# Kernel optimization log

Hardware: AMD Instinct MI355X
Metric: run time of the kernel (lower is better)

## Reference

```python
import jax, jax.numpy as jnp
import numpy as np

B, S, D = 4, 2048, 1024
H, HD = 16, 64
DFF = 4096
EPS = 1e-6


def setup_inputs() -> dict:
    key = jax.random.key(0)
    ks = jax.random.split(key, 16)
    sc = 0.02
    def w(k, shape):
        return jax.random.normal(k, shape, dtype=jnp.float32) * sc
    return {
        'x': jax.random.normal(ks[0], (B, S, D), dtype=jnp.float32),
        'wq': w(ks[1], (D, D)), 'bq': jnp.zeros((D,), jnp.float32),
        'wk': w(ks[2], (D, D)), 'bk': jnp.zeros((D,), jnp.float32),
        'wv': w(ks[3], (D, D)), 'bv': jnp.zeros((D,), jnp.float32),
        'wo': w(ks[4], (D, D)), 'bo': jnp.zeros((D,), jnp.float32),
        'w1': w(ks[5], (D, DFF)), 'b1': jnp.zeros((DFF,), jnp.float32),
        'w2': w(ks[6], (DFF, D)), 'b2': jnp.zeros((D,), jnp.float32),
        'ln1_a': jnp.ones((D,), jnp.float32), 'ln1_b': jnp.zeros((D,), jnp.float32),
        'ln2_a': jnp.ones((D,), jnp.float32), 'ln2_b': jnp.zeros((D,), jnp.float32),
    }


def layernorm(x, alpha, bias):
    # Matches torch module: std is unbiased (ddof=1), divide by (std + eps)
    mean = jnp.mean(x, axis=-1, keepdims=True)
    var = jnp.sum((x - mean) ** 2, axis=-1, keepdims=True) / (x.shape[-1] - 1)
    std = jnp.sqrt(var)
    return alpha * ((x - mean) / (std + EPS)) + bias


def mha(x, wq, bq, wk, bk, wv, bv, wo, bo):
    q = (x @ wq + bq).reshape(B, S, H, HD)
    k = (x @ wk + bk).reshape(B, S, H, HD)
    v = (x @ wv + bv).reshape(B, S, H, HD)
    scores = jnp.einsum('bqhd,bkhd->bhqk', q, k) / jnp.sqrt(jnp.float32(HD))
    attn = jax.nn.softmax(scores, axis=-1)
    out = jnp.einsum('bhqk,bkhd->bqhd', attn, v).reshape(B, S, D)
    return out @ wo + bo


def reference(x, wq, bq, wk, bk, wv, bv, wo, bo, w1, b1, w2, b2,
              ln1_a, ln1_b, ln2_a, ln2_b):
    # Residual 1: x + MHA(LN(x))   (dropout = identity, eval mode)
    x = x + mha(layernorm(x, ln1_a, ln1_b), wq, bq, wk, bk, wv, bv, wo, bo)
    # Residual 2: x + FFN(LN(x))
    h = layernorm(x, ln2_a, ln2_b)
    ffn = jax.nn.relu(h @ w1 + b1) @ w2 + b2
    return x + ffn
```

## Files before the change

### kernel.cpp

```cpp
#include <hip/hip_runtime.h>

#define S_ 2048
#define D_ 1024

typedef unsigned short u16;
typedef unsigned int u32;
typedef __bf16 bf16x8 __attribute__((ext_vector_type(8)));
typedef unsigned short us8 __attribute__((ext_vector_type(8)));
typedef unsigned short us4 __attribute__((ext_vector_type(4)));
typedef unsigned int u32x4 __attribute__((ext_vector_type(4)));
typedef float f32x4 __attribute__((ext_vector_type(4)));

#if __has_builtin(__builtin_amdgcn_exp2f)
#define EXP2(x) __builtin_amdgcn_exp2f(x)
#else
#define EXP2(x) exp2f(x)
#endif

static __device__ __forceinline__ u16 f2bf(float f) {
  unsigned u = __builtin_bit_cast(unsigned, f);
  u += 0x7fffu + ((u >> 16) & 1u);
  return (u16)(u >> 16);
}

static __device__ __forceinline__ float bf2f(u16 h) {
  return __builtin_bit_cast(float, (u32)h << 16);
}

static __device__ __forceinline__ unsigned cvtpk_bf16(float lo, float hi) {
  unsigned r;
  asm("v_cvt_pk_bf16_f32 %0, %1, %2" : "=v"(r) : "v"(lo), "v"(hi));
  return r;
}

static __device__ __forceinline__ f32x4 mfma16(bf16x8 a, bf16x8 b, f32x4 c) {
  return __builtin_amdgcn_mfma_f32_16x16x32_bf16(a, b, c, 0, 0, 0);
}

static __device__ __forceinline__ void gload16(const void* g, void* lds) {
  __builtin_amdgcn_global_load_lds((const __attribute__((address_space(1))) void*)g,
                                   (__attribute__((address_space(3))) void*)lds, 16, 0, 0);
}

__global__ __launch_bounds__(256) void prep_kernel(
    const float* __restrict__ x, u16* __restrict__ xA, const float* __restrict__ ln1a,
    const float* __restrict__ ln1b, const float* __restrict__ wq, const float* __restrict__ wk,
    const float* __restrict__ wv, const float* __restrict__ wo, const float* __restrict__ w1,
    const float* __restrict__ w2, const float* __restrict__ bq, const float* __restrict__ bk,
    const float* __restrict__ bv, u16* __restrict__ wqkv, u16* __restrict__ wot,
    u16* __restrict__ w1t, u16* __restrict__ w2t, float* __restrict__ bcat, float qs) {
  const int bid = blockIdx.x;
  const int tx = threadIdx.x, ty = threadIdx.y;
  const int tid = ty * 32 + tx;
  if (bid < 8192) {
    const int row = bid;
    const float4 v = *(const float4*)(x + (size_t)row * D_ + tid * 4);
    float s = v.x + v.y + v.z + v.w;
    float ss = v.x * v.x + v.y * v.y + v.z * v.z + v.w * v.w;
#pragma unroll
    for (int off = 32; off >= 1; off >>= 1) {
      s += __shfl_xor(s, off);
      ss += __shfl_xor(ss, off);
    }
    __shared__ float red[8];
    const int w = tid >> 6, lane = tid & 63;
    if (lane == 0) { red[w] = s; red[4 + w] = ss; }
    __syncthreads();
    s = red[0] + red[1] + red[2] + red[3];
    ss = red[4] + red[5] + red[6] + red[7];
    const float mean = s * (1.0f / D_);
    const float var = (ss - s * mean) * (1.0f / (D_ - 1));
    const float inv = 1.0f / (sqrtf(var) + 1e-6f);
    const int j = tid * 4;
    const float4 av = *(const float4*)(ln1a + j);
    const float4 bv = *(const float4*)(ln1b + j);
    us4 o;
    o[0] = f2bf((v.x - mean) * inv * av.x + bv.x);
    o[1] = f2bf((v.y - mean) * inv * av.y + bv.y);
    o[2] = f2bf((v.z - mean) * inv * av.z + bv.z);
    o[3] = f2bf((v.w - mean) * inv * av.w + bv.w);
    *(us4*)(xA + (size_t)row * D_ + j) = o;
    return;
  }
  if (bid >= 20480) {
    const int i = (bid - 20480) * 256 + tid;
    bcat[i] = (i < 1024) ? bq[i] * qs : ((i < 2048) ? bk[i - 1024] : bv[i - 2048]);
    return;
  }
  const int tb = bid - 8192;
  const float* in;
  u16* out;
  int K, N, idx;
  float sc = 1.0f;
  if (tb < 4096) {
    K = 1024; N = 1024; idx = tb & 1023;
    if (tb < 1024)      { in = wq; out = wqkv;             sc = qs; }
    else if (tb < 2048) { in = wk; out = wqkv + (1 << 20); }
    else if (tb < 3072) { in = wv; out = wqkv + (2 << 20); }
    else                { in = wo; out = wot; }
  } else if (tb < 8192) {
    in = w1; out = w1t; K = 1024; N = 4096; idx = tb - 4096;
  } else {
    in = w2; out = w2t; K = 4096; N = 1024; idx = tb - 8192;
  }
  const int nb = N >> 5;
  const int n0 = (idx % nb) * 32, k0 = (idx / nb) * 32;
  __shared__ float t[32][33];
#pragma unroll
  for (int i = 0; i < 4; i++)
    t[ty + 8 * i][tx] = in[(size_t)(k0 + ty + 8 * i) * N + n0 + tx];
  __syncthreads();
#pragma unroll
  for (int i = 0; i < 4; i++)
    out[(size_t)(n0 + ty + 8 * i) * K + k0 + tx] = f2bf(t[tx][ty + 8 * i] * sc);
}

__global__ __launch_bounds__(256) void ln_bf16_kernel(const u16* __restrict__ in,
                                                      u16* __restrict__ out,
                                                      const float* __restrict__ alpha,
                                                      const float* __restrict__ beta) {
  const int row = blockIdx.x;
  const int tid = threadIdx.x;
  const us4 h = *(const us4*)(in + (size_t)row * D_ + tid * 4);
  float v0 = bf2f(h[0]), v1 = bf2f(h[1]), v2 = bf2f(h[2]), v3 = bf2f(h[3]);
  float s = v0 + v1 + v2 + v3;
  float ss = v0 * v0 + v1 * v1 + v2 * v2 + v3 * v3;
#pragma unroll
  for (int off = 32; off >= 1; off >>= 1) {
    s += __shfl_xor(s, off);
    ss += __shfl_xor(ss, off);
  }
  __shared__ float red[8];
  const int w = tid >> 6, lane = tid & 63;
  if (lane == 0) { red[w] = s; red[4 + w] = ss; }
  __syncthreads();
  s = red[0] + red[1] + red[2] + red[3];
  ss = red[4] + red[5] + red[6] + red[7];
  const float mean = s * (1.0f / D_);
  const float var = (ss - s * mean) * (1.0f / (D_ - 1));
  const float inv = 1.0f / (sqrtf(var) + 1e-6f);
  const int j = tid * 4;
  const float4 av = *(const float4*)(alpha + j);
  const float4 bv = *(const float4*)(beta + j);
  us4 o;
  o[0] = f2bf((v0 - mean) * inv * av.x + bv.x);
  o[1] = f2bf((v1 - mean) * inv * av.y + bv.y);
  o[2] = f2bf((v2 - mean) * inv * av.z + bv.z);
  o[3] = f2bf((v3 - mean) * inv * av.w + bv.w);
  *(us4*)(out + (size_t)row * D_ + j) = o;
}

template <int OM, int RESID>
__global__ __launch_bounds__(256, 2) void gemm_bt128(const u16* __restrict__ A,
                                                     const u16* __restrict__ Bt,
                                                     const float* __restrict__ bias,
                                                     const void* __restrict__ resid,
                                                     void* __restrict__ outp, int N, int K) {
  __shared__ u16 lds[2 * 16384];
  const int tid = threadIdx.x;
  const int lane = tid & 63, w = tid >> 6;
  const int g = lane >> 4, r = lane & 15;
  const int wr = w >> 1, wc = w & 1;
  const int gx = gridDim.x;
  const int nwg = gx * gridDim.y;
  const int orig = blockIdx.y * gx + blockIdx.x;
  const int nid = (orig & 7) * (nwg >> 3) + (orig >> 3);
  const int bx = nid % gx, by = nid / gx;
  const size_t row0 = (size_t)by * 128;
  const int col0 = bx * 128;

  float bias4[4];
#pragma unroll
  for (int n = 0; n < 4; n++) bias4[n] = bias[col0 + wc * 64 + n * 16 + r];

  f32x4 acc[4][4];
#pragma unroll
  for (int m = 0; m < 4; m++)
#pragma unroll
    for (int n = 0; n < 4; n++) {
      f32x4 z = {bias4[n], bias4[n], bias4[n], bias4[n]};
      acc[m][n] = z;
    }

  const int lrow = tid >> 3;
  const int scol = 8 * ((tid & 7) ^ (lrow & 7));
  const u16* gA = A + (row0 + lrow) * (size_t)K + scol;
  const u16* gB = Bt + ((size_t)col0 + lrow) * (size_t)K + scol;
  const int nt = K >> 6;
  const int sw = (r & 7) << 3;

  {
    u16* d = lds + w * 512;
#pragma unroll
    for (int j = 0; j < 4; j++) gload16(gA + (size_t)(j * 32) * K, d + j * 2048);
#pragma unroll
    for (int j = 0; j < 4; j++) gload16(gB + (size_t)(j * 32) * K, d + 8192 + j * 2048);
  }

  for (int t = 0; t < nt; ++t) {
    const u16* As_ = lds + (t & 1) * 16384;
    const u16* Bs_ = As_ + 8192;
    if (t + 1 < nt) {
      u16* d = lds + ((t + 1) & 1) * 16384 + w * 512;
      const size_t ko = (size_t)(t + 1) * 64;
#pragma unroll
      for (int j = 0; j < 4; j++) gload16(gA + (size_t)(j * 32) * K + ko, d + j * 2048);
#pragma unroll
      for (int j = 0; j < 4; j++) gload16(gB + (size_t)(j * 32) * K + ko, d + 8192 + j * 2048);
      asm volatile("s_waitcnt vmcnt(8)" ::: "memory");
    } else {
      asm volatile("s_waitcnt vmcnt(0)" ::: "memory");
    }
    __builtin_amdgcn_s_barrier();
    asm volatile("" ::: "memory");

    bf16x8 bfr[2][4];
#pragma unroll
    for (int kk = 0; kk < 2; kk++)
#pragma unroll
      for (int n = 0; n < 4; n++)
        bfr[kk][n] = __builtin_bit_cast(
            bf16x8, *(const us8*)(Bs_ + (wc * 64 + n * 16 + r) * 64 + ((kk * 32 + g * 8) ^ sw)));

#pragma unroll
    for (int p = 0; p < 4; ++p) {
      const int row = wr * 64 + p * 16 + r;
      bf16x8 a0 = __builtin_bit_cast(bf16x8, *(const us8*)(As_ + row * 64 + ((g * 8) ^ sw)));
      bf16x8 a1 = __builtin_bit_cast(bf16x8, *(const us8*)(As_ + row * 64 + ((32 + g * 8) ^ sw)));
      asm volatile("" ::: "memory");
      if (p > 0) __builtin_amdgcn_s_barrier();
      asm volatile("s_waitcnt lgkmcnt(0)" ::: "memory");
      __builtin_amdgcn_sched_barrier(0);
      __builtin_amdgcn_s_setprio(1);
#pragma unroll
      for (int n = 0; n < 4; n++) {
        acc[p][n] = mfma16(a0, bfr[0][n], acc[p][n]);
        acc[p][n] = mfma16(a1, bfr[1][n], acc[p][n]);
      }
      __builtin_amdgcn_s_setprio(0);
    }
    asm volatile("" ::: "memory");
    __builtin_amdgcn_s_barrier();
  }

#pragma unroll
  for (int m = 0; m < 4; m++)
#pragma unroll
    for (int n = 0; n < 4; n++)
#pragma unroll
      for (int i = 0; i < 4; i++) {
        const size_t rg = row0 + wr * 64 + m * 16 + 4 * g + i;
        const int cg = col0 + wc * 64 + n * 16 + r;
        float v = acc[m][n][i];
        if (RESID == 1) v += ((const float*)resid)[rg * N + cg];
        if (RESID == 2) v += bf2f(((const u16*)resid)[rg * N + cg]);
        if (OM == 1)
          ((float*)outp)[rg * N + cg] = v;
        else
          ((u16*)outp)[rg * N + cg] = f2bf(v);
      }
}

template <int OM, bool RELU>
__global__ __launch_bounds__(512, 2) void gemm_bt256(const u16* __restrict__ A,
                                                     const u16* __restrict__ Bt,
                                                     const float* __restrict__ bias,
                                                     void* __restrict__ outp,
                                                     void* __restrict__ out1,
                                                     void* __restrict__ out2, int N, int K) {
  __shared__ u16 lds[2 * 32768];
  const int tid = threadIdx.x;
  const int lane = tid & 63, w = tid >> 6;
  const int g = lane >> 4, r = lane & 15;
  const int wr = w >> 2, wc = w & 3;
  const int gx = gridDim.x;
  const int nwg = gx * gridDim.y;
  const int orig = blockIdx.y * gx + blockIdx.x;
  const int nid = (orig & 7) * (nwg >> 3) + (orig >> 3);
  const int bx = nid % gx, by = nid / gx;
  const size_t row0 = (size_t)by * 256;
  const int col0 = bx * 256;

  float bias4[4];
#pragma unroll
  for (int n = 0; n < 4; n++) bias4[n] = bias[col0 + wc * 64 + n * 16 + r];

  f32x4 acc[8][4];
#pragma unroll
  for (int m = 0; m < 8; m++)
#pragma unroll
    for (int n = 0; n < 4; n++) {
      f32x4 z = {bias4[n], bias4[n], bias4[n], bias4[n]};
      acc[m][n] = z;
    }

  const int lrow = tid >> 3;
  const int scol = 8 * ((tid & 7) ^ (lrow & 7));
  const u16* gA = A + (row0 + lrow) * (size_t)K + scol;
  const u16* gB = Bt + ((size_t)col0 + lrow) * (size_t)K + scol;
  const int nt = K >> 6;
  const int sw = (r & 7) << 3;

  {
    u16* d = lds + w * 512;
#pragma unroll
    for (int j = 0; j < 4; j++) gload16(gA + (size_t)(j * 64) * K, d + j * 4096);
#pragma unroll
    for (int j = 0; j < 4; j++) gload16(gB + (size_t)(j * 64) * K, d + 16384 + j * 4096);
  }

  for (int t = 0; t < nt; ++t) {
    const u16* As_ = lds + (t & 1) * 32768;
    const u16* Bs_ = As_ + 16384;
    if (t + 1 < nt) {
      u16* d = lds + ((t + 1) & 1) * 32768 + w * 512;
      const size_t ko = (size_t)(t + 1) * 64;
#pragma unroll
      for (int j = 0; j < 4; j++) gload16(gA + (size_t)(j * 64) * K + ko, d + j * 4096);
#pragma unroll
      for (int j = 0; j < 4; j++) gload16(gB + (size_t)(j * 64) * K + ko, d + 16384 + j * 4096);
      asm volatile("s_waitcnt vmcnt(8)" ::: "memory");
    } else {
      asm volatile("s_waitcnt vmcnt(0)" ::: "memory");
    }
    __builtin_amdgcn_s_barrier();
    asm volatile("" ::: "memory");

    bf16x8 bfr[2][4];
#pragma unroll
    for (int kk = 0; kk < 2; kk++)
#pragma unroll
      for (int n = 0; n < 4; n++)
        bfr[kk][n] = __builtin_bit_cast(
            bf16x8, *(const us8*)(Bs_ + (wc * 64 + n * 16 + r) * 64 + ((kk * 32 + g * 8) ^ sw)));

#pragma unroll
    for (int p = 0; p < 4; ++p) {
      bf16x8 af[2][2];
#pragma unroll
      for (int mm = 0; mm < 2; mm++) {
        const int row = wr * 128 + (p * 2 + mm) * 16 + r;
        af[0][mm] = __builtin_bit_cast(bf16x8, *(const us8*)(As_ + row * 64 + ((g * 8) ^ sw)));
        af[1][mm] =
            __builtin_bit_cast(bf16x8, *(const us8*)(As_ + row * 64 + ((32 + g * 8) ^ sw)));
      }
      asm volatile("" ::: "memory");
      if (p > 0) __builtin_amdgcn_s_barrier();
      asm volatile("s_waitcnt lgkmcnt(0)" ::: "memory");
      __builtin_amdgcn_sched_barrier(0);
      __builtin_amdgcn_s_setprio(1);
#pragma unroll
      for (int mm = 0; mm < 2; mm++)
#pragma unroll
        for (int n = 0; n < 4; n++) {
          acc[p * 2 + mm][n] = mfma16(af[0][mm], bfr[0][n], acc[p * 2 + mm][n]);
          acc[p * 2 + mm][n] = mfma16(af[1][mm], bfr[1][n], acc[p * 2 + mm][n]);
        }
      __builtin_amdgcn_s_setprio(0);
    }
    asm volatile("" ::: "memory");
    __builtin_amdgcn_s_barrier();
  }

#pragma unroll
  for (int m = 0; m < 8; m++)
#pragma unroll
    for (int n = 0; n < 4; n++) {
      if (OM == 2) {
        const int seg = col0 >> 10;
        const int cl = (col0 & 1023) + wc * 64 + n * 16 + r;
        if (seg == 2) {
          const int head = cl >> 6, hd = cl & 63;
          const size_t rg0 = row0 + wr * 128 + m * 16 + 4 * g;
          const int b = (int)(rg0 >> 11), s0 = (int)(rg0 & 2047);
          const int s0p = (s0 & ~63) | (s0 & 32) | ((s0 << 1) & 24) | ((s0 >> 2) & 4);
          us4 o;
#pragma unroll
          for (int i = 0; i < 4; i++) o[i] = f2bf(acc[m][n][i]);
          *(us4*)((u16*)out2 + (((size_t)(b * 16 + head) * 64 + hd) * S_ + s0p)) = o;
        } else {
          u16* dst = (u16*)(seg == 0 ? outp : out1);
#pragma unroll
          for (int i = 0; i < 4; i++) {
            const size_t rg = row0 + wr * 128 + m * 16 + 4 * g + i;
            dst[rg * D_ + cl] = f2bf(acc[m][n][i]);
          }
        }
      } else {
#pragma unroll
        for (int i = 0; i < 4; i++) {
          const size_t rg = row0 + wr * 128 + m * 16 + 4 * g + i;
          const int cg = col0 + wc * 64 + n * 16 + r;
          float v = acc[m][n][i];
          if (RELU) v = fmaxf(v, 0.0f);
          ((u16*)outp)[rg * N + cg] = f2bf(v);
        }
      }
    }
}

__global__ __launch_bounds__(512) void attn_kernel(const u16* __restrict__ Q,
                                                   const u16* __restrict__ Km,
                                                   const u16* __restrict__ Vt_g,
                                                   u16* __restrict__ O) {
  __shared__ u16 Klds[2][2][4096];
  __shared__ u16 Vlds[2][2][4096];
  const int tid = threadIdx.x;
  const int lane = tid & 63, w = tid >> 6;
  const int g = lane >> 4, r = lane & 15;
  const int orig = blockIdx.y * 8 + blockIdx.x;
  const int nid = (orig & 7) * 64 + (orig >> 3);
  const int qblk = nid & 7, bh = nid >> 3;
  const int b = bh >> 4, head = bh & 15;
  const size_t rowbase = (size_t)b * S_;
  const int colbase = head * 64;
  const int qw = qblk * 256 + w * 32;

  bf16x8 qf0[2], qf1[2];
#pragma unroll
  for (int qh = 0; qh < 2; qh++) {
    const u16* qrow = Q + (rowbase + qw + qh * 16 + r) * D_ + colbase;
    qf0[qh] = __builtin_bit_cast(bf16x8, *(const us8*)(qrow + g * 8));
    qf1[qh] = __builtin_bit_cast(bf16x8, *(const us8*)(qrow + 32 + g * 8));
  }

  const int srow = tid >> 3;
  const int sslot = (tid & 7) ^ (srow & 7);
  const u16* Kg = Km + (rowbase + srow) * D_ + colbase + sslot * 8;
  const u16* Vg = Vt_g + ((size_t)bh * 64 + srow) * S_ + sslot * 8;

  const us8 onesw = {0x3F80, 0x3F80, 0x3F80, 0x3F80, 0x3F80, 0x3F80, 0x3F80, 0x3F80};
  const bf16x8 ones8 = __builtin_bit_cast(bf16x8, onesw);

  f32x4 lacc[2];
  f32x4 oacc[2][4];
#pragma unroll
  for (int qh = 0; qh < 2; qh++) {
    f32x4 z = {0.0f, 0.0f, 0.0f, 0.0f};
    lacc[qh] = z;
#pragma unroll
    for (int n = 0; n < 4; n++) oacc[qh][n] = z;
  }

  constexpr int NG = S_ / 128;

#define STAGE_GRP(t, bq_)                                                            \
  {                                                                                  \
    const int _t = (t), _b = (bq_);                                                  \
    _Pragma("unroll") for (int h = 0; h < 2; h++) {                                  \
      gload16(Kg + (size_t)(_t * 128 + h * 64) * D_, (char*)&Klds[_b][h][0] + w * 1024); \
      gload16(Vg + _t * 128 + h * 64, (char*)&Vlds[_b][h][0] + w * 1024);            \
    }                                                                                \
  }

  STAGE_GRP(0, 0);

  for (int t = 0; t < NG; ++t) {
    const int buf = t & 1;
    if (t + 1 < NG) {
      STAGE_GRP(t + 1, buf ^ 1);
      asm volatile("s_waitcnt vmcnt(4)" ::: "memory");
    } else {
      asm volatile("s_waitcnt vmcnt(0)" ::: "memory");
    }
    __builtin_amdgcn_s_barrier();
    asm volatile("" ::: "memory");

    f32x4 st0[4][2];
    __builtin_amdgcn_s_setprio(1);
#pragma unroll
    for (int f = 0; f < 4; f++) {
      const int row = f * 16 + r;
      const int sw7 = row & 7;
      const u16* Kc = &Klds[buf][0][0];
      const bf16x8 k0 = __builtin_bit_cast(bf16x8, *(const us8*)(Kc + row * 64 + (g ^ sw7) * 8));
      const bf16x8 k1 =
          __builtin_bit_cast(bf16x8, *(const us8*)(Kc + row * 64 + ((g + 4) ^ sw7) * 8));
#pragma unroll
      for (int qh = 0; qh < 2; qh++) {
        f32x4 z = {0.0f, 0.0f, 0.0f, 0.0f};
        st0[f][qh] = mfma16(k0, qf0[qh], z);
        st0[f][qh] = mfma16(k1, qf1[qh], st0[f][qh]);
      }
    }
    __builtin_amdgcn_s_setprio(0);
    bf16x8 paA0[2], paA1[2];
#pragma unroll
    for (int qh = 0; qh < 2; qh++) {
      u32 pw[8];
#pragma unroll
      for (int f = 0; f < 4; f++) {
        const float e0 = EXP2(st0[f][qh][0]);
        const float e1 = EXP2(st0[f][qh][1]);
        const float e2 = EXP2(st0[f][qh][2]);
        const float e3 = EXP2(st0[f][qh][3]);
        pw[f * 2] = cvtpk_bf16(e0, e1);
        pw[f * 2 + 1] = cvtpk_bf16(e2, e3);
      }
      const u32x4 a0w = {pw[0], pw[1], pw[2], pw[3]};
      const u32x4 a1w = {pw[4], pw[5], pw[6], pw[7]};
      paA0[qh] = __builtin_bit_cast(bf16x8, a0w);
      paA1[qh] = __builtin_bit_cast(bf16x8, a1w);
    }
    f32x4 st1[4][2];
    __builtin_amdgcn_s_setprio(1);
#pragma unroll
    for (int f = 0; f < 4; f++) {
      const int row = f * 16 + r;
      const int sw7 = row & 7;
      const u16* Kc = &Klds[buf][1][0];
      const bf16x8 k0 = __builtin_bit_cast(bf16x8, *(const us8*)(Kc + row * 64 + (g ^ sw7) * 8));
      const bf16x8 k1 =
          __builtin_bit_cast(bf16x8, *(const us8*)(Kc + row * 64 + ((g + 4) ^ sw7) * 8));
#pragma unroll
      for (int qh = 0; qh < 2; qh++) {
        f32x4 z = {0.0f, 0.0f, 0.0f, 0.0f};
        st1[f][qh] = mfma16(k0, qf0[qh], z);
        st1[f][qh] = mfma16(k1, qf1[qh], st1[f][qh]);
      }
    }
#pragma unroll
    for (int qh = 0; qh < 2; qh++) {
      lacc[qh] = mfma16(paA0[qh], ones8, lacc[qh]);
      lacc[qh] = mfma16(paA1[qh], ones8, lacc[qh]);
    }
#pragma unroll
    for (int n = 0; n < 4; n++) {
      const int row = n * 16 + r;
      const int sw7 = r & 7;
      const u16* Vc = &Vlds[buf][0][0];
      const bf16x8 vb0 = __builtin_bit_cast(bf16x8, *(const us8*)(Vc + row * 64 + (g ^ sw7) * 8));
      const bf16x8 vb1 =
          __builtin_bit_cast(bf16x8, *(const us8*)(Vc + row * 64 + ((4 + g) ^ sw7) * 8));
#pragma unroll
      for (int qh = 0; qh < 2; qh++) {
        oacc[qh][n] = mfma16(paA0[qh], vb0, oacc[qh][n]);
        oacc[qh][n] = mfma16(paA1[qh], vb1, oacc[qh][n]);
      }
    }
    __builtin_amdgcn_s_setprio(0);
    bf16x8 paB0[2], paB1[2];
#pragma unroll
    for (int qh = 0; qh < 2; qh++) {
      u32 pw[8];
#pragma unroll
      for (int f = 0; f < 4; f++) {
        const float e0 = EXP2(st1[f][qh][0]);
        const float e1 = EXP2(st1[f][qh][1]);
        const float e2 = EXP2(st1[f][qh][2]);
        const float e3 = EXP2(st1[f][qh][3]);
        pw[f * 2] = cvtpk_bf16(e0, e1);
        pw[f * 2 + 1] = cvtpk_bf16(e2, e3);
      }
      const u32x4 a0w = {pw[0], pw[1], pw[2], pw[3]};
      const u32x4 a1w = {pw[4], pw[5], pw[6], pw[7]};
      paB0[qh] = __builtin_bit_cast(bf16x8, a0w);
      paB1[qh] = __builtin_bit_cast(bf16x8, a1w);
    }
    __builtin_amdgcn_s_setprio(1);
#pragma unroll
    for (int qh = 0; qh < 2; qh++) {
      lacc[qh] = mfma16(paB0[qh], ones8, lacc[qh]);
      lacc[qh] = mfma16(paB1[qh], ones8, lacc[qh]);
    }
#pragma unroll
    for (int n = 0; n < 4; n++) {
      const int row = n * 16 + r;
      const int sw7 = r & 7;
      const u16* Vc = &Vlds[buf][1][0];
      const bf16x8 vb0 = __builtin_bit_cast(bf16x8, *(const us8*)(Vc + row * 64 + (g ^ sw7) * 8));
      const bf16x8 vb1 =
          __builtin_bit_cast(bf16x8, *(const us8*)(Vc + row * 64 + ((4 + g) ^ sw7) * 8));
#pragma unroll
      for (int qh = 0; qh < 2; qh++) {
        oacc[qh][n] = mfma16(paB0[qh], vb0, oacc[qh][n]);
        oacc[qh][n] = mfma16(paB1[qh], vb1, oacc[qh][n]);
      }
    }
    __builtin_amdgcn_s_setprio(0);

    asm volatile("" ::: "memory");
    __builtin_amdgcn_s_barrier();
    asm volatile("" ::: "memory");
  }
#undef STAGE_GRP

#pragma unroll
  for (int qh = 0; qh < 2; qh++) {
    float ld[4];
#pragma unroll
    for (int i = 0; i < 4; i++) ld[i] = 1.0f / lacc[qh][i];
#pragma unroll
    for (int n = 0; n < 4; n++)
#pragma unroll
      for (int i = 0; i < 4; i++)
        O[(rowbase + qw + qh * 16 + 4 * g + i) * D_ + colbase + n * 16 + r] =
            f2bf(oacc[qh][n][i] * ld[i]);
  }
}

extern "C" void kernel_launch(void* const* d_in, const int* in_sizes, int n_in, void* d_out,
                              int out_size, void* d_ws, size_t ws_size, hipStream_t stream) {
  (void)in_sizes; (void)n_in; (void)out_size; (void)ws_size;
  const float* x = (const float*)d_in[0];
  const float* wq = (const float*)d_in[1];
  const float* bq = (const float*)d_in[2];
  const float* wk = (const float*)d_in[3];
  const float* bk = (const float*)d_in[4];
  const float* wv = (const float*)d_in[5];
  const float* bv = (const float*)d_in[6];
  const float* wo = (const float*)d_in[7];
  const float* bo = (const float*)d_in[8];
  const float* w1 = (const float*)d_in[9];
  const float* b1 = (const float*)d_in[10];
  const float* w2 = (const float*)d_in[11];
  const float* b2 = (const float*)d_in[12];
  const float* ln1a = (const float*)d_in[13];
  const float* ln1b = (const float*)d_in[14];
  const float* ln2a = (const float*)d_in[15];
  const float* ln2b = (const float*)d_in[16];

  char* ws = (char*)d_ws;
  const size_t MB = 1ull << 20;
  u16* wqkv = (u16*)(ws + 0 * MB);
  u16* wot = (u16*)(ws + 6 * MB);
  u16* w1t = (u16*)(ws + 8 * MB);
  u16* w2t = (u16*)(ws + 16 * MB);
  u16* xA = (u16*)(ws + 24 * MB);
  u16* qb = (u16*)(ws + 40 * MB);
  u16* kb = (u16*)(ws + 56 * MB);
  u16* vt = (u16*)(ws + 72 * MB);
  float* bcat = (float*)(ws + 88 * MB);
  u16* ff1 = (u16*)(ws + 40 * MB);
  u16* x1b = (u16*)(ws + 104 * MB);

  const float QSCALE = 0.125f * 1.4426950408889634f;

  prep_kernel<<<20492, dim3(32, 8), 0, stream>>>(x, xA, ln1a, ln1b, wq, wk, wv, wo, w1, w2, bq,
                                                 bk, bv, wqkv, wot, w1t, w2t, bcat, QSCALE);
  gemm_bt256<2, false><<<dim3(12, 32), 512, 0, stream>>>(xA, wqkv, bcat, qb, kb, vt, 3072, 1024);
  attn_kernel<<<dim3(8, 64), 512, 0, stream>>>(qb, kb, vt, xA);
  gemm_bt128<0, 1><<<dim3(8, 64), 256, 0, stream>>>(xA, wot, bo, x, x1b, 1024, 1024);
  ln_bf16_kernel<<<8192, 256, 0, stream>>>(x1b, xA, ln2a, ln2b);
  gemm_bt256<0, true><<<dim3(16, 32), 512, 0, stream>>>(xA, w1t, b1, ff1, nullptr, nullptr, 4096,
                                                        1024);
  gemm_bt128<1, 2><<<dim3(8, 64), 256, 0, stream>>>(ff1, w2t, b2, x1b, (float*)d_out, 1024, 4096);
}
```

Before: 331.9 us.

## Interleave next-tile loads with MFMA phases and widen weight transpose tiles

Both GEMM kernels now issue the next K-tile's global-to-LDS loads in pairs across the four MFMA sub-phases. They wait on partial vmcnt counts and use two barriers per iteration instead of one barrier per sub-phase plus a trailing one. B-tile loads are issued first and A-tile loads only after a mid-iteration barrier, so loads overlap compute and synchronisation is reduced. The weight transpose in the prep kernel moves to 64x32 tiles with float4 reads and 16-byte bf16 writes, halving the transpose block count. The new wait counts and barrier placement must still keep double-buffer reuse race-free.

```diff
diff --git a/kernel.cpp b/kernel.cpp
--- a/kernel.cpp
+++ b/kernel.cpp
@@ -50,8 +50,7 @@
     const float* __restrict__ bv, u16* __restrict__ wqkv, u16* __restrict__ wot,
     u16* __restrict__ w1t, u16* __restrict__ w2t, float* __restrict__ bcat, float qs) {
   const int bid = blockIdx.x;
-  const int tx = threadIdx.x, ty = threadIdx.y;
-  const int tid = ty * 32 + tx;
+  const int tid = threadIdx.y * 32 + threadIdx.x;
   if (bid < 8192) {
     const int row = bid;
     const float4 v = *(const float4*)(x + (size_t)row * D_ + tid * 4);
@@ -82,8 +81,8 @@
     *(us4*)(xA + (size_t)row * D_ + j) = o;
     return;
   }
-  if (bid >= 20480) {
-    const int i = (bid - 20480) * 256 + tid;
+  if (bid >= 14336) {
+    const int i = (bid - 14336) * 256 + tid;
     bcat[i] = (i < 1024) ? bq[i] * qs : ((i < 2048) ? bk[i - 1024] : bv[i - 2048]);
     return;
   }
@@ -92,27 +91,32 @@
   u16* out;
   int K, N, idx;
   float sc = 1.0f;
-  if (tb < 4096) {
-    K = 1024; N = 1024; idx = tb & 1023;
-    if (tb < 1024)      { in = wq; out = wqkv;             sc = qs; }
-    else if (tb < 2048) { in = wk; out = wqkv + (1 << 20); }
-    else if (tb < 3072) { in = wv; out = wqkv + (2 << 20); }
-    else                { in = wo; out = wot; }
-  } else if (tb < 8192) {
-    in = w1; out = w1t; K = 1024; N = 4096; idx = tb - 4096;
+  if (tb < 2048) {
+    K = 1024; N = 1024; idx = tb & 511;
+    if (tb < 512)        { in = wq; out = wqkv;             sc = qs; }
+    else if (tb < 1024)  { in = wk; out = wqkv + (1 << 20); }
+    else if (tb < 1536)  { in = wv; out = wqkv + (2 << 20); }
+    else                 { in = wo; out = wot; }
+  } else if (tb < 4096) {
+    in = w1; out = w1t; K = 1024; N = 4096; idx = tb - 2048;
   } else {
-    in = w2; out = w2t; K = 4096; N = 1024; idx = tb - 8192;
-  }
-  const int nb = N >> 5;
-  const int n0 = (idx % nb) * 32, k0 = (idx / nb) * 32;
-  __shared__ float t[32][33];
-#pragma unroll
-  for (int i = 0; i < 4; i++)
-    t[ty + 8 * i][tx] = in[(size_t)(k0 + ty + 8 * i) * N + n0 + tx];
+    in = w2; out = w2t; K = 4096; N = 1024; idx = tb - 4096;
+  }
+  const int nk = K >> 6;
+  const int k0 = (idx % nk) * 64, n0 = (idx / nk) * 32;
+  __shared__ float t[32][65];
+  const int kk = tid >> 2, nj = (tid & 3) * 8;
+  const float* src = in + (size_t)(k0 + kk) * N + n0 + nj;
+  const float4 v0 = *(const float4*)(src);
+  const float4 v1 = *(const float4*)(src + 4);
+  t[nj + 0][kk] = v0.x; t[nj + 1][kk] = v0.y; t[nj + 2][kk] = v0.z; t[nj + 3][kk] = v0.w;
+  t[nj + 4][kk] = v1.x; t[nj + 5][kk] = v1.y; t[nj + 6][kk] = v1.z; t[nj + 7][kk] = v1.w;
   __syncthreads();
-#pragma unroll
-  for (int i = 0; i < 4; i++)
-    out[(size_t)(n0 + ty + 8 * i) * K + k0 + tx] = f2bf(t[tx][ty + 8 * i] * sc);
+  const int row = tid >> 3, kb = (tid & 7) * 8;
+  us8 o;
+#pragma unroll
+  for (int j = 0; j < 8; j++) o[j] = f2bf(t[row][kb + j] * sc);
+  *(us8*)(out + (size_t)(n0 + row) * K + k0 + kb) = o;
 }
 
 __global__ __launch_bounds__(256) void ln_bf16_kernel(const u16* __restrict__ in,
@@ -191,44 +195,66 @@
 
   {
     u16* d = lds + w * 512;
-#pragma unroll
-    for (int j = 0; j < 4; j++) gload16(gA + (size_t)(j * 32) * K, d + j * 2048);
-#pragma unroll
-    for (int j = 0; j < 4; j++) gload16(gB + (size_t)(j * 32) * K, d + 8192 + j * 2048);
+    gload16(gB, d + 8192);
+    gload16(gB + (size_t)32 * K, d + 10240);
+    gload16(gB + (size_t)64 * K, d + 12288);
+    gload16(gB + (size_t)96 * K, d + 14336);
+    gload16(gA, d);
+    gload16(gA + (size_t)64 * K, d + 4096);
+    gload16(gA + (size_t)32 * K, d + 2048);
+    gload16(gA + (size_t)96 * K, d + 6144);
   }
 
   for (int t = 0; t < nt; ++t) {
     const u16* As_ = lds + (t & 1) * 16384;
     const u16* Bs_ = As_ + 8192;
-    if (t + 1 < nt) {
-      u16* d = lds + ((t + 1) & 1) * 16384 + w * 512;
-      const size_t ko = (size_t)(t + 1) * 64;
-#pragma unroll
-      for (int j = 0; j < 4; j++) gload16(gA + (size_t)(j * 32) * K + ko, d + j * 2048);
-#pragma unroll
-      for (int j = 0; j < 4; j++) gload16(gB + (size_t)(j * 32) * K + ko, d + 8192 + j * 2048);
-      asm volatile("s_waitcnt vmcnt(8)" ::: "memory");
-    } else {
-      asm volatile("s_waitcnt vmcnt(0)" ::: "memory");
-    }
-    __builtin_amdgcn_s_barrier();
-    asm volatile("" ::: "memory");
+    const bool st = (t + 1 < nt);
+    u16* d = lds + ((t + 1) & 1) * 16384 + w * 512;
+    const size_t ko = (size_t)(t + 1) * 64;
 
     bf16x8 bfr[2][4];
 #pragma unroll
-    for (int kk = 0; kk < 2; kk++)
-#pragma unroll
-      for (int n = 0; n < 4; n++)
-        bfr[kk][n] = __builtin_bit_cast(
-            bf16x8, *(const us8*)(Bs_ + (wc * 64 + n * 16 + r) * 64 + ((kk * 32 + g * 8) ^ sw)));
-
-#pragma unroll
     for (int p = 0; p < 4; ++p) {
+      if (p == 0) {
+        asm volatile("s_waitcnt vmcnt(2)" ::: "memory");
+        __builtin_amdgcn_s_barrier();
+        asm volatile("" ::: "memory");
+        if (st) {
+          gload16(gB + ko, d + 8192);
+          gload16(gB + (size_t)32 * K + ko, d + 10240);
+        }
+#pragma unroll
+        for (int kk = 0; kk < 2; kk++)
+#pragma unroll
+          for (int n = 0; n < 4; n++)
+            bfr[kk][n] = __builtin_bit_cast(
+                bf16x8,
+                *(const us8*)(Bs_ + (wc * 64 + n * 16 + r) * 64 + ((kk * 32 + g * 8) ^ sw)));
+      } else if (p == 1) {
+        if (st) {
+          gload16(gB + (size_t)64 * K + ko, d + 12288);
+          gload16(gB + (size_t)96 * K + ko, d + 14336);
+        }
+      } else if (p == 2) {
+        if (st)
+          asm volatile("s_waitcnt vmcnt(4)" ::: "memory");
+        else
+          asm volatile("s_waitcnt vmcnt(0)" ::: "memory");
+        __builtin_amdgcn_s_barrier();
+        asm volatile("" ::: "memory");
+        if (st) {
+          gload16(gA + ko, d);
+          gload16(gA + (size_t)64 * K + ko, d + 4096);
+        }
+      } else {
+        if (st) {
+          gload16(gA + (size_t)32 * K + ko, d + 2048);
+          gload16(gA + (size_t)96 * K + ko, d + 6144);
+        }
+      }
       const int row = wr * 64 + p * 16 + r;
       bf16x8 a0 = __builtin_bit_cast(bf16x8, *(const us8*)(As_ + row * 64 + ((g * 8) ^ sw)));
       bf16x8 a1 = __builtin_bit_cast(bf16x8, *(const us8*)(As_ + row * 64 + ((32 + g * 8) ^ sw)));
-      asm volatile("" ::: "memory");
-      if (p > 0) __builtin_amdgcn_s_barrier();
       asm volatile("s_waitcnt lgkmcnt(0)" ::: "memory");
       __builtin_amdgcn_sched_barrier(0);
       __builtin_amdgcn_s_setprio(1);
@@ -239,8 +265,6 @@
       }
       __builtin_amdgcn_s_setprio(0);
     }
-    asm volatile("" ::: "memory");
-    __builtin_amdgcn_s_barrier();
   }
 
 #pragma unroll
@@ -303,39 +327,63 @@
 
   {
     u16* d = lds + w * 512;
-#pragma unroll
-    for (int j = 0; j < 4; j++) gload16(gA + (size_t)(j * 64) * K, d + j * 4096);
-#pragma unroll
-    for (int j = 0; j < 4; j++) gload16(gB + (size_t)(j * 64) * K, d + 16384 + j * 4096);
+    gload16(gB, d + 16384);
+    gload16(gB + (size_t)64 * K, d + 20480);
+    gload16(gB + (size_t)128 * K, d + 24576);
+    gload16(gB + (size_t)192 * K, d + 28672);
+    gload16(gA, d);
+    gload16(gA + (size_t)128 * K, d + 8192);
+    gload16(gA + (size_t)64 * K, d + 4096);
+    gload16(gA + (size_t)192 * K, d + 12288);
   }
 
   for (int t = 0; t < nt; ++t) {
     const u16* As_ = lds + (t & 1) * 32768;
     const u16* Bs_ = As_ + 16384;
-    if (t + 1 < nt) {
-      u16* d = lds + ((t + 1) & 1) * 32768 + w * 512;
-      const size_t ko = (size_t)(t + 1) * 64;
-#pragma unroll
-      for (int j = 0; j < 4; j++) gload16(gA + (size_t)(j * 64) * K + ko, d + j * 4096);
-#pragma unroll
-      for (int j = 0; j < 4; j++) gload16(gB + (size_t)(j * 64) * K + ko, d + 16384 + j * 4096);
-      asm volatile("s_waitcnt vmcnt(8)" ::: "memory");
-    } else {
-      asm volatile("s_waitcnt vmcnt(0)" ::: "memory");
-    }
-    __builtin_amdgcn_s_barrier();
-    asm volatile("" ::: "memory");
+    const bool st = (t + 1 < nt);
+    u16* d = lds + ((t + 1) & 1) * 32768 + w * 512;
+    const size_t ko = (size_t)(t + 1) * 64;
 
     bf16x8 bfr[2][4];
 #pragma unroll
-    for (int kk = 0; kk < 2; kk++)
-#pragma unroll
-      for (int n = 0; n < 4; n++)
-        bfr[kk][n] = __builtin_bit_cast(
-            bf16x8, *(const us8*)(Bs_ + (wc * 64 + n * 16 + r) * 64 + ((kk * 32 + g * 8) ^ sw)));
-
-#pragma unroll
     for (int p = 0; p < 4; ++p) {
+      if (p == 0) {
+        asm volatile("s_waitcnt vmcnt(2)" ::: "memory");
+        __builtin_amdgcn_s_barrier();
+        asm volatile("" ::: "memory");
+        if (st) {
+          gload16(gB + ko, d + 16384);
+          gload16(gB + (size_t)64 * K + ko, d + 20480);
+        }
+#pragma unroll
+        for (int kk = 0; kk < 2; kk++)
+#pragma unroll
+          for (int n = 0; n < 4; n++)
+            bfr[kk][n] = __builtin_bit_cast(
+                bf16x8,
+                *(const us8*)(Bs_ + (wc * 64 + n * 16 + r) * 64 + ((kk * 32 + g * 8) ^ sw)));
+      } else if (p == 1) {
+        if (st) {
+          gload16(gB + (size_t)128 * K + ko, d + 24576);
+          gload16(gB + (size_t)192 * K + ko, d + 28672);
+        }
+      } else if (p == 2) {
+        if (st)
+          asm volatile("s_waitcnt vmcnt(4)" ::: "memory");
+        else
+          asm volatile("s_waitcnt vmcnt(0)" ::: "memory");
+        __builtin_amdgcn_s_barrier();
+        asm volatile("" ::: "memory");
+        if (st) {
+          gload16(gA + ko, d);
+          gload16(gA + (size_t)128 * K + ko, d + 8192);
+        }
+      } else {
+        if (st) {
+          gload16(gA + (size_t)64 * K + ko, d + 4096);
+          gload16(gA + (size_t)192 * K + ko, d + 12288);
+        }
+      }
       bf16x8 af[2][2];
 #pragma unroll
       for (int mm = 0; mm < 2; mm++) {
@@ -344,8 +392,6 @@
         af[1][mm] =
             __builtin_bit_cast(bf16x8, *(const us8*)(As_ + row * 64 + ((32 + g * 8) ^ sw)));
       }
-      asm volatile("" ::: "memory");
-      if (p > 0) __builtin_amdgcn_s_barrier();
       asm volatile("s_waitcnt lgkmcnt(0)" ::: "memory");
       __builtin_amdgcn_sched_barrier(0);
       __builtin_amdgcn_s_setprio(1);
@@ -358,8 +404,6 @@
         }
       __builtin_amdgcn_s_setprio(0);
     }
-    asm volatile("" ::: "memory");
-    __builtin_amdgcn_s_barrier();
   }
 
 #pragma unroll
@@ -636,7 +680,7 @@
 
   const float QSCALE = 0.125f * 1.4426950408889634f;
 
-  prep_kernel<<<20492, dim3(32, 8), 0, stream>>>(x, xA, ln1a, ln1b, wq, wk, wv, wo, w1, w2, bq,
+  prep_kernel<<<14348, dim3(32, 8), 0, stream>>>(x, xA, ln1a, ln1b, wq, wk, wv, wo, w1, w2, bq,
                                                  bk, bv, wqkv, wot, w1t, w2t, bcat, QSCALE);
   gemm_bt256<2, false><<<dim3(12, 32), 512, 0, stream>>>(xA, wqkv, bcat, qb, kb, vt, 3072, 1024);
   attn_kernel<<<dim3(8, 64), 512, 0, stream>>>(qb, kb, vt, xA);
```

New measurement: 335.5 us. No clear change (+1.1%).

## Switch GEMMs to 32x32x16 MFMA and widen weight transpose tiles

Applied to the files above, without the earlier changes.

Both GEMM kernels move from 16x16x32 bf16 MFMA to 32x32x16 MFMA with f32x16 accumulators. The LDS fragment loads and the epilogue row/column mapping are rewritten for the 32-lane layout, including the transposed V store. Larger MFMA tiles cut the number of LDS fragment reads per FLOP and issue fewer, longer matrix instructions. Separately, the weight transpose in prep_kernel now handles 64x32 tiles with float4 loads and 16-byte bf16 stores, which halves its block count and widens its memory accesses. The risks are extra LDS bank conflicts from the new access pattern and a mistake in the epilogue index mapping.

```diff
diff --git a/kernel.cpp b/kernel.cpp
--- a/kernel.cpp
+++ b/kernel.cpp
@@ -10,6 +10,7 @@
 typedef unsigned short us4 __attribute__((ext_vector_type(4)));
 typedef unsigned int u32x4 __attribute__((ext_vector_type(4)));
 typedef float f32x4 __attribute__((ext_vector_type(4)));
+typedef float f32x16 __attribute__((ext_vector_type(16)));
 
 #if __has_builtin(__builtin_amdgcn_exp2f)
 #define EXP2(x) __builtin_amdgcn_exp2f(x)
@@ -35,6 +36,10 @@
 
 static __device__ __forceinline__ f32x4 mfma16(bf16x8 a, bf16x8 b, f32x4 c) {
   return __builtin_amdgcn_mfma_f32_16x16x32_bf16(a, b, c, 0, 0, 0);
+}
+
+static __device__ __forceinline__ f32x16 mfma32(bf16x8 a, bf16x8 b, f32x16 c) {
+  return __builtin_amdgcn_mfma_f32_32x32x16_bf16(a, b, c, 0, 0, 0);
 }
 
 static __device__ __forceinline__ void gload16(const void* g, void* lds) {
@@ -50,8 +55,7 @@
     const float* __restrict__ bv, u16* __restrict__ wqkv, u16* __restrict__ wot,
     u16* __restrict__ w1t, u16* __restrict__ w2t, float* __restrict__ bcat, float qs) {
   const int bid = blockIdx.x;
-  const int tx = threadIdx.x, ty = threadIdx.y;
-  const int tid = ty * 32 + tx;
+  const int tid = threadIdx.y * 32 + threadIdx.x;
   if (bid < 8192) {
     const int row = bid;
     const float4 v = *(const float4*)(x + (size_t)row * D_ + tid * 4);
@@ -82,8 +86,8 @@
     *(us4*)(xA + (size_t)row * D_ + j) = o;
     return;
   }
-  if (bid >= 20480) {
-    const int i = (bid - 20480) * 256 + tid;
+  if (bid >= 14336) {
+    const int i = (bid - 14336) * 256 + tid;
     bcat[i] = (i < 1024) ? bq[i] * qs : ((i < 2048) ? bk[i - 1024] : bv[i - 2048]);
     return;
   }
@@ -92,27 +96,32 @@
   u16* out;
   int K, N, idx;
   float sc = 1.0f;
-  if (tb < 4096) {
-    K = 1024; N = 1024; idx = tb & 1023;
-    if (tb < 1024)      { in = wq; out = wqkv;             sc = qs; }
-    else if (tb < 2048) { in = wk; out = wqkv + (1 << 20); }
-    else if (tb < 3072) { in = wv; out = wqkv + (2 << 20); }
-    else                { in = wo; out = wot; }
-  } else if (tb < 8192) {
-    in = w1; out = w1t; K = 1024; N = 4096; idx = tb - 4096;
+  if (tb < 2048) {
+    K = 1024; N = 1024; idx = tb & 511;
+    if (tb < 512)        { in = wq; out = wqkv;             sc = qs; }
+    else if (tb < 1024)  { in = wk; out = wqkv + (1 << 20); }
+    else if (tb < 1536)  { in = wv; out = wqkv + (2 << 20); }
+    else                 { in = wo; out = wot; }
+  } else if (tb < 4096) {
+    in = w1; out = w1t; K = 1024; N = 4096; idx = tb - 2048;
   } else {
-    in = w2; out = w2t; K = 4096; N = 1024; idx = tb - 8192;
-  }
-  const int nb = N >> 5;
-  const int n0 = (idx % nb) * 32, k0 = (idx / nb) * 32;
-  __shared__ float t[32][33];
-#pragma unroll
-  for (int i = 0; i < 4; i++)
-    t[ty + 8 * i][tx] = in[(size_t)(k0 + ty + 8 * i) * N + n0 + tx];
+    in = w2; out = w2t; K = 4096; N = 1024; idx = tb - 4096;
+  }
+  const int nk = K >> 6;
+  const int k0 = (idx % nk) * 64, n0 = (idx / nk) * 32;
+  __shared__ float t[32][65];
+  const int kk = tid >> 2, nj = (tid & 3) * 8;
+  const float* src = in + (size_t)(k0 + kk) * N + n0 + nj;
+  const float4 v0 = *(const float4*)(src);
+  const float4 v1 = *(const float4*)(src + 4);
+  t[nj + 0][kk] = v0.x; t[nj + 1][kk] = v0.y; t[nj + 2][kk] = v0.z; t[nj + 3][kk] = v0.w;
+  t[nj + 4][kk] = v1.x; t[nj + 5][kk] = v1.y; t[nj + 6][kk] = v1.z; t[nj + 7][kk] = v1.w;
   __syncthreads();
-#pragma unroll
-  for (int i = 0; i < 4; i++)
-    out[(size_t)(n0 + ty + 8 * i) * K + k0 + tx] = f2bf(t[tx][ty + 8 * i] * sc);
+  const int row = tid >> 3, kb = (tid & 7) * 8;
+  us8 o;
+#pragma unroll
+  for (int j = 0; j < 8; j++) o[j] = f2bf(t[row][kb + j] * sc);
+  *(us8*)(out + (size_t)(n0 + row) * K + k0 + kb) = o;
 }
 
 __global__ __launch_bounds__(256) void ln_bf16_kernel(const u16* __restrict__ in,
@@ -159,7 +168,7 @@
   __shared__ u16 lds[2 * 16384];
   const int tid = threadIdx.x;
   const int lane = tid & 63, w = tid >> 6;
-  const int g = lane >> 4, r = lane & 15;
+  const int l31 = lane & 31, hi = lane >> 5;
   const int wr = w >> 1, wc = w & 1;
   const int gx = gridDim.x;
   const int nwg = gx * gridDim.y;
@@ -169,25 +178,23 @@
   const size_t row0 = (size_t)by * 128;
   const int col0 = bx * 128;
 
-  float bias4[4];
-#pragma unroll
-  for (int n = 0; n < 4; n++) bias4[n] = bias[col0 + wc * 64 + n * 16 + r];
-
-  f32x4 acc[4][4];
-#pragma unroll
-  for (int m = 0; m < 4; m++)
-#pragma unroll
-    for (int n = 0; n < 4; n++) {
-      f32x4 z = {bias4[n], bias4[n], bias4[n], bias4[n]};
-      acc[m][n] = z;
-    }
+  float biasv[2];
+#pragma unroll
+  for (int n = 0; n < 2; n++) biasv[n] = bias[col0 + wc * 64 + n * 32 + l31];
+
+  f32x16 acc[2][2];
+#pragma unroll
+  for (int m = 0; m < 2; m++)
+#pragma unroll
+    for (int n = 0; n < 2; n++)
+#pragma unroll
+      for (int q = 0; q < 16; q++) acc[m][n][q] = biasv[n];
 
   const int lrow = tid >> 3;
   const int scol = 8 * ((tid & 7) ^ (lrow & 7));
   const u16* gA = A + (row0 + lrow) * (size_t)K + scol;
   const u16* gB = Bt + ((size_t)col0 + lrow) * (size_t)K + scol;
   const int nt = K >> 6;
-  const int sw = (r & 7) << 3;
 
   {
     u16* d = lds + w * 512;
@@ -214,29 +221,34 @@
     __builtin_amdgcn_s_barrier();
     asm volatile("" ::: "memory");
 
-    bf16x8 bfr[2][4];
-#pragma unroll
-    for (int kk = 0; kk < 2; kk++)
-#pragma unroll
-      for (int n = 0; n < 4; n++)
-        bfr[kk][n] = __builtin_bit_cast(
-            bf16x8, *(const us8*)(Bs_ + (wc * 64 + n * 16 + r) * 64 + ((kk * 32 + g * 8) ^ sw)));
+    bf16x8 bfr[4][2];
+#pragma unroll
+    for (int ks = 0; ks < 4; ks++)
+#pragma unroll
+      for (int n = 0; n < 2; n++) {
+        const int row = wc * 64 + n * 32 + l31;
+        bfr[ks][n] = __builtin_bit_cast(
+            bf16x8, *(const us8*)(Bs_ + row * 64 + (((ks * 2 + hi) ^ (row & 7)) << 3)));
+      }
 
 #pragma unroll
     for (int p = 0; p < 4; ++p) {
-      const int row = wr * 64 + p * 16 + r;
-      bf16x8 a0 = __builtin_bit_cast(bf16x8, *(const us8*)(As_ + row * 64 + ((g * 8) ^ sw)));
-      bf16x8 a1 = __builtin_bit_cast(bf16x8, *(const us8*)(As_ + row * 64 + ((32 + g * 8) ^ sw)));
+      bf16x8 af[2];
+#pragma unroll
+      for (int m = 0; m < 2; m++) {
+        const int row = wr * 64 + m * 32 + l31;
+        af[m] = __builtin_bit_cast(
+            bf16x8, *(const us8*)(As_ + row * 64 + (((p * 2 + hi) ^ (row & 7)) << 3)));
+      }
       asm volatile("" ::: "memory");
       if (p > 0) __builtin_amdgcn_s_barrier();
       asm volatile("s_waitcnt lgkmcnt(0)" ::: "memory");
       __builtin_amdgcn_sched_barrier(0);
       __builtin_amdgcn_s_setprio(1);
 #pragma unroll
-      for (int n = 0; n < 4; n++) {
-        acc[p][n] = mfma16(a0, bfr[0][n], acc[p][n]);
-        acc[p][n] = mfma16(a1, bfr[1][n], acc[p][n]);
-      }
+      for (int m = 0; m < 2; m++)
+#pragma unroll
+        for (int n = 0; n < 2; n++) acc[m][n] = mfma32(af[m], bfr[p][n], acc[m][n]);
       __builtin_amdgcn_s_setprio(0);
     }
     asm volatile("" ::: "memory");
@@ -244,14 +256,14 @@
   }
 
 #pragma unroll
-  for (int m = 0; m < 4; m++)
-#pragma unroll
-    for (int n = 0; n < 4; n++)
-#pragma unroll
-      for (int i = 0; i < 4; i++) {
-        const size_t rg = row0 + wr * 64 + m * 16 + 4 * g + i;
-        const int cg = col0 + wc * 64 + n * 16 + r;
-        float v = acc[m][n][i];
+  for (int m = 0; m < 2; m++)
+#pragma unroll
+    for (int n = 0; n < 2; n++) {
+      const int cg = col0 + wc * 64 + n * 32 + l31;
+#pragma unroll
+      for (int q = 0; q < 16; q++) {
+        const size_t rg = row0 + wr * 64 + m * 32 + (q & 3) + 8 * (q >> 2) + 4 * hi;
+        float v = acc[m][n][q];
         if (RESID == 1) v += ((const float*)resid)[rg * N + cg];
         if (RESID == 2) v += bf2f(((const u16*)resid)[rg * N + cg]);
         if (OM == 1)
@@ -259,6 +271,7 @@
         else
           ((u16*)outp)[rg * N + cg] = f2bf(v);
       }
+    }
 }
 
 template <int OM, bool RELU>
@@ -271,7 +284,7 @@
   __shared__ u16 lds[2 * 32768];
   const int tid = threadIdx.x;
   const int lane = tid & 63, w = tid >> 6;
-  const int g = lane >> 4, r = lane & 15;
+  const int l31 = lane & 31, hi = lane >> 5;
   const int wr = w >> 2, wc = w & 3;
   const int gx = gridDim.x;
   const int nwg = gx * gridDim.y;
@@ -281,25 +294,23 @@
   const size_t row0 = (size_t)by * 256;
   const int col0 = bx * 256;
 
-  float bias4[4];
-#pragma unroll
-  for (int n = 0; n < 4; n++) bias4[n] = bias[col0 + wc * 64 + n * 16 + r];
-
-  f32x4 acc[8][4];
-#pragma unroll
-  for (int m = 0; m < 8; m++)
-#pragma unroll
-    for (int n = 0; n < 4; n++) {
-      f32x4 z = {bias4[n], bias4[n], bias4[n], bias4[n]};
-      acc[m][n] = z;
-    }
+  float biasv[2];
+#pragma unroll
+  for (int n = 0; n < 2; n++) biasv[n] = bias[col0 + wc * 64 + n * 32 + l31];
+
+  f32x16 acc[4][2];
+#pragma unroll
+  for (int m = 0; m < 4; m++)
+#pragma unroll
+    for (int n = 0; n < 2; n++)
+#pragma unroll
+      for (int q = 0; q < 16; q++) acc[m][n][q] = biasv[n];
 
   const int lrow = tid >> 3;
   const int scol = 8 * ((tid & 7) ^ (lrow & 7));
   const u16* gA = A + (row0 + lrow) * (size_t)K + scol;
   const u16* gB = Bt + ((size_t)col0 + lrow) * (size_t)K + scol;
   const int nt = K >> 6;
-  const int sw = (r & 7) << 3;
 
   {
     u16* d = lds + w * 512;
@@ -326,23 +337,24 @@
     __builtin_amdgcn_s_barrier();
     asm volatile("" ::: "memory");
 
-    bf16x8 bfr[2][4];
-#pragma unroll
-    for (int kk = 0; kk < 2; kk++)
-#pragma unroll
-      for (int n = 0; n < 4; n++)
-        bfr[kk][n] = __builtin_bit_cast(
-            bf16x8, *(const us8*)(Bs_ + (wc * 64 + n * 16 + r) * 64 + ((kk * 32 + g * 8) ^ sw)));
+    bf16x8 bfr[4][2];
+#pragma unroll
+    for (int ks = 0; ks < 4; ks++)
+#pragma unroll
+      for (int n = 0; n < 2; n++) {
+        const int row = wc * 64 + n * 32 + l31;
+        bfr[ks][n] = __builtin_bit_cast(
+            bf16x8, *(const us8*)(Bs_ + row * 64 + (((ks * 2 + hi) ^ (row & 7)) << 3)));
+      }
 
 #pragma unroll
     for (int p = 0; p < 4; ++p) {
-      bf16x8 af[2][2];
-#pragma unroll
-      for (int mm = 0; mm < 2; mm++) {
-        const int row = wr * 128 + (p * 2 + mm) * 16 + r;
-        af[0][mm] = __builtin_bit_cast(bf16x8, *(const us8*)(As_ + row * 64 + ((g * 8) ^ sw)));
-        af[1][mm] =
-            __builtin_bit_cast(bf16x8, *(const us8*)(As_ + row * 64 + ((32 + g * 8) ^ sw)));
+      bf16x8 af[4];
+#pragma unroll
+      for (int m = 0; m < 4; m++) {
+        const int row = wr * 128 + m * 32 + l31;
+        af[m] = __builtin_bit_cast(
+            bf16x8, *(const us8*)(As_ + row * 64 + (((p * 2 + hi) ^ (row & 7)) << 3)));
       }
       asm volatile("" ::: "memory");
       if (p > 0) __builtin_amdgcn_s_barrier();
@@ -350,12 +362,9 @@
       __builtin_amdgcn_sched_barrier(0);
       __builtin_amdgcn_s_setprio(1);
 #pragma unroll
-      for (int mm = 0; mm < 2; mm++)
-#pragma unroll
-        for (int n = 0; n < 4; n++) {
-          acc[p * 2 + mm][n] = mfma16(af[0][mm], bfr[0][n], acc[p * 2 + mm][n]);
-          acc[p * 2 + mm][n] = mfma16(af[1][mm], bfr[1][n], acc[p * 2 + mm][n]);
-        }
+      for (int m = 0; m < 4; m++)
+#pragma unroll
+        for (int n = 0; n < 2; n++) acc[m][n] = mfma32(af[m], bfr[p][n], acc[m][n]);
       __builtin_amdgcn_s_setprio(0);
     }
     asm volatile("" ::: "memory");
@@ -363,35 +372,38 @@
   }
 
 #pragma unroll
-  for (int m = 0; m < 8; m++)
-#pragma unroll
-    for (int n = 0; n < 4; n++) {
+  for (int m = 0; m < 4; m++)
+#pragma unroll
+    for (int n = 0; n < 2; n++) {
       if (OM == 2) {
         const int seg = col0 >> 10;
-        const int cl = (col0 & 1023) + wc * 64 + n * 16 + r;
+        const int cl = (col0 & 1023) + wc * 64 + n * 32 + l31;
         if (seg == 2) {
           const int head = cl >> 6, hd = cl & 63;
-          const size_t rg0 = row0 + wr * 128 + m * 16 + 4 * g;
-          const int b = (int)(rg0 >> 11), s0 = (int)(rg0 & 2047);
-          const int s0p = (s0 & ~63) | (s0 & 32) | ((s0 << 1) & 24) | ((s0 >> 2) & 4);
-          us4 o;
-#pragma unroll
-          for (int i = 0; i < 4; i++) o[i] = f2bf(acc[m][n][i]);
-          *(us4*)((u16*)out2 + (((size_t)(b * 16 + head) * 64 + hd) * S_ + s0p)) = o;
+#pragma unroll
+          for (int qq = 0; qq < 4; qq++) {
+            const size_t rg0 = row0 + wr * 128 + m * 32 + 8 * qq + 4 * hi;
+            const int b = (int)(rg0 >> 11), s0 = (int)(rg0 & 2047);
+            const int s0p = (s0 & ~63) | (s0 & 32) | ((s0 << 1) & 24) | ((s0 >> 2) & 4);
+            us4 o;
+#pragma unroll
+            for (int i = 0; i < 4; i++) o[i] = f2bf(acc[m][n][qq * 4 + i]);
+            *(us4*)((u16*)out2 + (((size_t)(b * 16 + head) * 64 + hd) * S_ + s0p)) = o;
+          }
         } else {
           u16* dst = (u16*)(seg == 0 ? outp : out1);
 #pragma unroll
-          for (int i = 0; i < 4; i++) {
-            const size_t rg = row0 + wr * 128 + m * 16 + 4 * g + i;
-            dst[rg * D_ + cl] = f2bf(acc[m][n][i]);
+          for (int q = 0; q < 16; q++) {
+            const size_t rg = row0 + wr * 128 + m * 32 + (q & 3) + 8 * (q >> 2) + 4 * hi;
+            dst[rg * D_ + cl] = f2bf(acc[m][n][q]);
           }
         }
       } else {
-#pragma unroll
-        for (int i = 0; i < 4; i++) {
-          const size_t rg = row0 + wr * 128 + m * 16 + 4 * g + i;
-          const int cg = col0 + wc * 64 + n * 16 + r;
-          float v = acc[m][n][i];
+        const int cg = col0 + wc * 64 + n * 32 + l31;
+#pragma unroll
+        for (int q = 0; q < 16; q++) {
+          const size_t rg = row0 + wr * 128 + m * 32 + (q & 3) + 8 * (q >> 2) + 4 * hi;
+          float v = acc[m][n][q];
           if (RELU) v = fmaxf(v, 0.0f);
           ((u16*)outp)[rg * N + cg] = f2bf(v);
         }
@@ -636,7 +648,7 @@
 
   const float QSCALE = 0.125f * 1.4426950408889634f;
 
-  prep_kernel<<<20492, dim3(32, 8), 0, stream>>>(x, xA, ln1a, ln1b, wq, wk, wv, wo, w1, w2, bq,
+  prep_kernel<<<14348, dim3(32, 8), 0, stream>>>(x, xA, ln1a, ln1b, wq, wk, wv, wo, w1, w2, bq,
                                                  bk, bv, wqkv, wot, w1t, w2t, bcat, QSCALE);
   gemm_bt256<2, false><<<dim3(12, 32), 512, 0, stream>>>(xA, wqkv, bcat, qb, kb, vt, 3072, 1024);
   attn_kernel<<<dim3(8, 64), 512, 0, stream>>>(qb, kb, vt, xA);
```

Result: slower. 345.0 us (+4.0%).
